# Kernel optimization log

Measured on AMD Instinct MI355X. Metric: run time of the kernel, lower is better.

Reference implementation:

```python
import jax, jax.numpy as jnp
import numpy as np

D = 512          # hidden_dim
H_HEADS = 8
DH = D // H_HEADS  # 64
L = 6            # n_layers
P = 8            # patch size
KT = 3           # temporal kernel
Z_DIM = 32
FILM_SCALE = 0.5
ROPE_BASE = 10000.0
EPS = 1e-5


def layer_norm(x, g, b):
    mu = x.mean(-1, keepdims=True)
    var = ((x - mu) ** 2).mean(-1, keepdims=True)
    return (x - mu) * jax.lax.rsqrt(var + EPS) * g + b


def rotate_half(x):
    x1, x2 = jnp.split(x, 2, axis=-1)
    return jnp.concatenate([-x2, x1], axis=-1)


def rope_time(T, dtype):
    half = DH // 2
    inv_freq = ROPE_BASE ** (-(jnp.arange(half, dtype=dtype) / half))  # (half,)
    angles = jnp.arange(T, dtype=dtype)[:, None] * inv_freq[None, :]   # (T, half)
    sin = jnp.concatenate([jnp.sin(angles), jnp.sin(angles)], -1)      # (T, DH)
    cos = jnp.concatenate([jnp.cos(angles), jnp.cos(angles)], -1)
    return sin, cos


def setup_inputs() -> dict:
    key = jax.random.key(0)
    ks = iter(jax.random.split(key, 64))
    n = lambda shape, s=0.02: jax.random.normal(next(ks), shape, jnp.float32) * s
    inp = {
        "x": jax.random.normal(next(ks), (16, 32, 3, 64, 64), jnp.float32),
        "z": jax.random.normal(next(ks), (16, 32, Z_DIM), jnp.float32),
        # tokenizer: CausalConv3d (kt,ph,pw)=(3,8,8), stride (1,8,8)
        "conv_w": n((D, 3, KT, P, P)),
        "conv_b": jnp.zeros((D,), jnp.float32),
        "tok_g": jnp.ones((D,), jnp.float32),
        "tok_b": jnp.zeros((D,), jnp.float32),
        # FiLM from z -> (gamma, beta)
        "film_w": n((Z_DIM, 2 * D)),
        "film_b": jnp.zeros((2 * D,), jnp.float32),
        # transformer blocks (stacked over L)
        "ln1_g": jnp.ones((L, D), jnp.float32), "ln1_b": jnp.zeros((L, D), jnp.float32),
        "kqv_w": n((L, D, 3 * D)), "kqv_b": jnp.zeros((L, 3 * D), jnp.float32),
        "proj_w": n((L, D, D)), "proj_b": jnp.zeros((L, D), jnp.float32),
        "ln2_g": jnp.ones((L, D), jnp.float32), "ln2_b": jnp.zeros((L, D), jnp.float32),
        "mlp_w1": n((L, D, 4 * D)), "mlp_b1": jnp.zeros((L, 4 * D), jnp.float32),
        "mlp_w2": n((L, 4 * D, D)), "mlp_b2": jnp.zeros((L, D), jnp.float32),
        "rs_attn": jnp.full((L,), 0.5, jnp.float32),
        "rs_mlp": jnp.full((L,), 0.5, jnp.float32),
        # scoring head
        "head_g": jnp.ones((D,), jnp.float32), "head_b": jnp.zeros((D,), jnp.float32),
        "head_w": n((D, 1)), "head_bias": jnp.zeros((1,), jnp.float32),
    }
    return inp


def _forward(x, z, conv_w, conv_b, tok_g, tok_b, film_w, film_b,
             ln1_g, ln1_b, kqv_w, kqv_b, proj_w, proj_b, ln2_g, ln2_b,
             mlp_w1, mlp_b1, mlp_w2, mlp_b2, rs_attn, rs_mlp,
             head_g, head_b, head_w, head_bias):
    B, T, C, Himg, Wimg = x.shape
    # ---- SpatialTemporalTokenizer: causal Conv3d (pad time on past only) ----
    xc = jnp.transpose(x, (0, 2, 1, 3, 4))  # [B,C,T,H,W]
    y = jax.lax.conv_general_dilated(
        xc, conv_w, window_strides=(1, P, P),
        padding=[(KT - 1, 0), (0, 0), (0, 0)],
        dimension_numbers=("NCDHW", "OIDHW", "NCDHW"))
    y = y + conv_b[None, :, None, None, None]          # [B,D,T,Hn,Wn]
    Hn, Wn = y.shape[3], y.shape[4]
    tok = jnp.transpose(y, (0, 2, 3, 4, 1)).reshape(B, T, Hn * Wn, D)
    tok = layer_norm(tok, tok_g, tok_b)                 # [B,T,N,D]
    # ---- FiLM conditioning from z ----
    gb = z @ film_w + film_b                            # [B,T,2D]
    gamma, beta = jnp.split(gb, 2, axis=-1)
    tok = (1.0 + FILM_SCALE * gamma)[:, :, None, :] * tok + (FILM_SCALE * beta)[:, :, None, :]
    # ---- spatial pooling -> temporal sequence ----
    h = tok.mean(axis=2)                                # [B,T,D]
    # ---- transformer stack (causal, time RoPE, pre-LN, gated residuals) ----
    sin_t, cos_t = rope_time(T, h.dtype)                # (T, DH)
    causal = jnp.tril(jnp.ones((T, T), bool))
    neg_inf = jnp.finfo(h.dtype).min
    for i in range(L):
        xi = layer_norm(h, ln1_g[i], ln1_b[i])
        kqv = xi @ kqv_w[i] + kqv_b[i]                  # [B,T,3D]
        k, q, v = jnp.split(kqv, 3, axis=-1)            # torch chunk order: k,q,v
        sh = lambda t: t.reshape(B, T, H_HEADS, DH).transpose(0, 2, 1, 3)  # [B,h,T,d]
        q, k, v = sh(q), sh(k), sh(v)
        q = q * cos_t + rotate_half(q) * sin_t
        k = k * cos_t + rotate_half(k) * sin_t
        att = jnp.einsum("bhqd,bhkd->bhqk", q, k) / np.sqrt(DH)
        att = jnp.where(causal[None, None], att, neg_inf)
        att = jax.nn.softmax(att, axis=-1)
        yv = jnp.einsum("bhqk,bhkd->bhqd", att, v)
        yv = yv.transpose(0, 2, 1, 3).reshape(B, T, D)
        attn_out = yv @ proj_w[i] + proj_b[i]
        h = h + rs_attn[i] * attn_out
        x2 = layer_norm(h, ln2_g[i], ln2_b[i])
        m = jax.nn.gelu(x2 @ mlp_w1[i] + mlp_b1[i], approximate=False) @ mlp_w2[i] + mlp_b2[i]
        h = h + rs_mlp[i] * m
    # ---- per-timestep score head ----
    h = layer_norm(h, head_g, head_b)
    score = (h @ head_w + head_bias)[..., 0]            # [B,T]
    return score


def reference(x, z, conv_w, conv_b, tok_g, tok_b, film_w, film_b,
              ln1_g, ln1_b, kqv_w, kqv_b, proj_w, proj_b, ln2_g, ln2_b,
              mlp_w1, mlp_b1, mlp_w2, mlp_b2, rs_attn, rs_mlp,
              head_g, head_b, head_w, head_bias):
    return _forward(x, z, conv_w, conv_b, tok_g, tok_b, film_w, film_b,
                    ln1_g, ln1_b, kqv_w, kqv_b, proj_w, proj_b, ln2_g, ln2_b,
                    mlp_w1, mlp_b1, mlp_w2, mlp_b2, rs_attn, rs_mlp,
                    head_g, head_b, head_w, head_bias)
```

## Files before the change

kernel.cpp:

```cpp
#include <hip/hip_runtime.h>
#include <math.h>

#define EPS 1e-5f

typedef __attribute__((ext_vector_type(8))) short short8;
typedef __attribute__((ext_vector_type(4))) float f32x4;

__device__ __forceinline__ short f2bf(float f) {
    unsigned u = __float_as_uint(f);
    u += 0x7fffu + ((u >> 16) & 1u);
    return (short)(u >> 16);
}
__device__ __forceinline__ float bf2f(short s) {
    return __uint_as_float(((unsigned)(unsigned short)s) << 16);
}
__device__ __forceinline__ void async16(const void* g, void* l) {
    __builtin_amdgcn_global_load_lds(
        (const __attribute__((address_space(1))) unsigned*)g,
        (__attribute__((address_space(3))) unsigned*)l, 16, 0, 0);
}

__device__ __forceinline__ float block_reduce_sum_256(float v, float* red) {
    #pragma unroll
    for (int o = 32; o > 0; o >>= 1) v += __shfl_down(v, o, 64);
    __syncthreads();
    if ((threadIdx.x & 63) == 0) red[threadIdx.x >> 6] = v;
    __syncthreads();
    return red[0] + red[1] + red[2] + red[3];
}

__global__ __launch_bounds__(256) void prep_all(
    const float* __restrict__ z, const float* __restrict__ fw,
    const float* __restrict__ fb, float* __restrict__ gb,
    const float* __restrict__ conv_w, short* __restrict__ wbf,
    const float* __restrict__ x, short* __restrict__ xbf,
    float* __restrict__ ropeS, float* __restrict__ ropeC,
    const float* __restrict__ kqv_w, short* __restrict__ kqvT,
    const float* __restrict__ proj_w, short* __restrict__ projT,
    const float* __restrict__ mlp_w1, short* __restrict__ mlp1T,
    const float* __restrict__ mlp_w2, short* __restrict__ mlp2T) {
    int bi = blockIdx.x, tid = threadIdx.x;
    if (bi < 512) {
        __shared__ float zs[32];
        if (tid < 32) zs[tid] = z[bi * 32 + tid];
        __syncthreads();
        for (int j = tid; j < 1024; j += 256) {
            float acc = fb[j];
            #pragma unroll
            for (int k = 0; k < 32; k++) acc = fmaf(zs[k], fw[k * 1024 + j], acc);
            gb[bi * 1024 + j] = acc;
        }
        return;
    }
    if (bi < 1664) {
        int i = (bi - 512) * 256 + tid;
        wbf[i] = f2bf(conv_w[i]);
        return;
    }
    if (bi < 4736) {
        int i = (bi - 1664) * 256 + tid;
        float4 a = *(const float4*)(x + (size_t)i * 8);
        float4 b = *(const float4*)(x + (size_t)i * 8 + 4);
        short8 o = {f2bf(a.x), f2bf(a.y), f2bf(a.z), f2bf(a.w),
                    f2bf(b.x), f2bf(b.y), f2bf(b.z), f2bf(b.w)};
        *(short8*)(xbf + (size_t)i * 8) = o;
        return;
    }
    if (bi < 4740) {
        int idx = (bi - 4736) * 256 + tid;
        if (idx < 1024) {
            int t = idx >> 5, j = idx & 31;
            float ang = (float)t * expf(-(float)j * (logf(10000.f) / 32.f));
            ropeS[idx] = sinf(ang);
            ropeC[idx] = cosf(ang);
        }
        return;
    }
    __shared__ float tile[32][33];
    int rel0 = bi - 4740;
    const float* src; short* dst; int NT, K, N, rel;
    if (rel0 < 4608)       { src = kqv_w;  dst = kqvT;  NT = 48; K = 512;  N = 1536; rel = rel0; }
    else if (rel0 < 6144)  { src = proj_w; dst = projT; NT = 16; K = 512;  N = 512;  rel = rel0 - 4608; }
    else if (rel0 < 12288) { src = mlp_w1; dst = mlp1T; NT = 64; K = 512;  N = 2048; rel = rel0 - 6144; }
    else                   { src = mlp_w2; dst = mlp2T; NT = 16; K = 2048; N = 512;  rel = rel0 - 12288; }
    int per = NT * (K / 32);
    int layer = rel / per, r2 = rel - layer * per;
    int nt = r2 % NT, kt = r2 / NT;
    src += (size_t)layer * K * N;
    dst += (size_t)layer * N * K;
    int n0 = nt * 32, k0 = kt * 32;
    int lx = tid & 31, ly = tid >> 5;
    #pragma unroll
    for (int i = 0; i < 32; i += 8)
        tile[ly + i][lx] = src[(size_t)(k0 + ly + i) * N + n0 + lx];
    __syncthreads();
    if (tid < 128) {
        int row = tid >> 2, c = tid & 3;
        short8 o;
        #pragma unroll
        for (int j = 0; j < 8; j++) o[j] = f2bf(tile[c * 8 + j][row]);
        *(short8*)(dst + (size_t)(n0 + row) * K + k0 + c * 8) = o;
    }
}

__global__ __launch_bounds__(256, 2) void conv_fused(
    const short* __restrict__ xbf, const short* __restrict__ wbf,
    const float* __restrict__ cb, const float* __restrict__ tg,
    const float* __restrict__ tb, const float* __restrict__ gb,
    float* __restrict__ h) {
    __shared__ short As[64 * 32];
    __shared__ short Bs[512 * 32];
    __shared__ float redsum[4][64], redss[4][64];
    __shared__ float mu_s[64], inv_s[64];
    int bt = blockIdx.x, b = bt >> 5, t = bt & 31;
    int tid = threadIdx.x;
    int wave = tid >> 6, lane = tid & 63, quad = lane >> 4, l16 = lane & 15;

    int rowA = tid >> 2;
    int cA = (tid & 3) ^ ((rowA >> 1) & 3);
    int hn = rowA >> 3, wn2 = rowA & 7;
    long long baseA = (((long long)(b * 32 + t - 2) * 3) << 12)
                      + (long long)(hn * 8) * 64 + wn2 * 8;

    f32x4 acc[4][8];
    #pragma unroll
    for (int mt = 0; mt < 4; mt++)
        #pragma unroll
        for (int nt = 0; nt < 8; nt++) acc[mt][nt] = (f32x4){0.f, 0.f, 0.f, 0.f};

    for (int k0 = 0; k0 < 576; k0 += 32) {
        #pragma unroll
        for (int e = 0; e < 8; e++) {
            int s = e * 256 + tid;
            int n = s >> 2;
            int c = (s & 3) ^ ((n >> 1) & 3);
            async16(wbf + (size_t)n * 576 + k0 + c * 8, Bs + s * 8);
        }
        {
            int ks = (k0 >> 3) + cA;
            int ch = (ks >= 24) + (ks >= 48);
            int r = ks - ch * 24;
            int kt = r >> 3, ph = r & 7;
            short8 v8 = (short8){0, 0, 0, 0, 0, 0, 0, 0};
            if (t + kt >= 2)
                v8 = *(const short8*)(xbf + baseA
                        + ((long long)(kt * 3 + ch) << 12) + ph * 64);
            *(short8*)(As + tid * 8) = v8;
        }
        __syncthreads();
        short8 af[4], bf[8];
        #pragma unroll
        for (int mt = 0; mt < 4; mt++) {
            int row = mt * 16 + l16;
            int pc = quad ^ ((row >> 1) & 3);
            af[mt] = *(const short8*)(As + row * 32 + pc * 8);
        }
        #pragma unroll
        for (int nt = 0; nt < 8; nt++) {
            int row = wave * 128 + nt * 16 + l16;
            int pc = quad ^ ((row >> 1) & 3);
            bf[nt] = *(const short8*)(Bs + row * 32 + pc * 8);
        }
        #pragma unroll
        for (int mt = 0; mt < 4; mt++)
            #pragma unroll
            for (int nt = 0; nt < 8; nt++)
                acc[mt][nt] = __builtin_amdgcn_mfma_f32_16x16x32_bf16(
                    af[mt], bf[nt], acc[mt][nt], 0, 0, 0);
        __syncthreads();
    }

    float cbn[8], tgn[8], tbn[8], Gn[8], Ben[8];
    #pragma unroll
    for (int nt = 0; nt < 8; nt++) {
        int n = wave * 128 + nt * 16 + l16;
        cbn[nt] = cb[n]; tgn[nt] = tg[n]; tbn[nt] = tb[n];
        Gn[nt]  = 1.f + 0.5f * gb[bt * 1024 + n];
        Ben[nt] = 0.5f * gb[bt * 1024 + 512 + n];
    }
    #pragma unroll
    for (int mt = 0; mt < 4; mt++)
        #pragma unroll
        for (int reg = 0; reg < 4; reg++) {
            float s = 0.f, ss = 0.f;
            #pragma unroll
            for (int nt = 0; nt < 8; nt++) {
                float v = acc[mt][nt][reg] + cbn[nt];
                s += v; ss += v * v;
            }
            #pragma unroll
            for (int o = 1; o < 16; o <<= 1) {
                s  += __shfl_xor(s, o, 64);
                ss += __shfl_xor(ss, o, 64);
            }
            if (l16 == 0) {
                int m = mt * 16 + quad * 4 + reg;
                redsum[wave][m] = s; redss[wave][m] = ss;
            }
        }
    __syncthreads();
    if (tid < 64) {
        float S  = redsum[0][tid] + redsum[1][tid] + redsum[2][tid] + redsum[3][tid];
        float SS = redss[0][tid] + redss[1][tid] + redss[2][tid] + redss[3][tid];
        float mu = S * (1.f / 512.f);
        float var = SS * (1.f / 512.f) - mu * mu;
        mu_s[tid] = mu; inv_s[tid] = rsqrtf(var + EPS);
    }
    __syncthreads();
    float hacc[8] = {0.f, 0.f, 0.f, 0.f, 0.f, 0.f, 0.f, 0.f};
    #pragma unroll
    for (int mt = 0; mt < 4; mt++)
        #pragma unroll
        for (int reg = 0; reg < 4; reg++) {
            int m = mt * 16 + quad * 4 + reg;
            float mu = mu_s[m], inv = inv_s[m];
            #pragma unroll
            for (int nt = 0; nt < 8; nt++) {
                float v = acc[mt][nt][reg] + cbn[nt];
                hacc[nt] += (v - mu) * inv;
            }
        }
    #pragma unroll
    for (int nt = 0; nt < 8; nt++) {
        hacc[nt] += __shfl_xor(hacc[nt], 16, 64);
        hacc[nt] += __shfl_xor(hacc[nt], 32, 64);
    }
    if (quad == 0)
        #pragma unroll
        for (int nt = 0; nt < 8; nt++) {
            int n = wave * 128 + nt * 16 + l16;
            h[bt * 512 + n] = Gn[nt] * (tgn[nt] * (hacc[nt] * (1.f / 64.f)) + tbn[nt])
                              + Ben[nt];
        }
}

__global__ __launch_bounds__(256) void attn_fused(
    const float* __restrict__ hsrc, const float* __restrict__ lng,
    const float* __restrict__ lnb, const short* __restrict__ Bw,
    const float* __restrict__ bias, const float* __restrict__ ropeS,
    const float* __restrict__ ropeC, short* __restrict__ yv) {
    __shared__ char smem[57344] __attribute__((aligned(16)));
    __shared__ float mu_s[32], inv_s[32];
    short* As = (short*)smem;
    short* BsB[2] = {(short*)(smem + 32768), (short*)(smem + 45056)};
    float (*qsf)[64] = (float(*)[64])(smem);
    float (*ksf)[64] = (float(*)[64])(smem + 8192);
    short* vT  = (short*)(smem + 16384);
    short* qrb = (short*)(smem + 20480);
    short* krb = (short*)(smem + 24576);
    float (*att)[33] = (float(*)[33])(smem + 28672);
    short* pA  = (short*)(smem + 36864);
    int blk = blockIdx.x, b = blk >> 3, hh = blk & 7;
    int tid = threadIdx.x;
    int m0 = b * 32;
    {
        int row = tid >> 3, l8 = tid & 7;
        const float* hp = hsrc + (size_t)(m0 + row) * 512 + l8 * 64;
        float s = 0.f, ss = 0.f;
        #pragma unroll
        for (int i = 0; i < 16; i++) {
            float4 v = *(const float4*)(hp + i * 4);
            s += v.x + v.y + v.z + v.w;
            ss += v.x * v.x + v.y * v.y + v.z * v.z + v.w * v.w;
        }
        s += __shfl_xor(s, 1, 64); ss += __shfl_xor(ss, 1, 64);
        s += __shfl_xor(s, 2, 64); ss += __shfl_xor(ss, 2, 64);
        s += __shfl_xor(s, 4, 64); ss += __shfl_xor(ss, 4, 64);
        if (l8 == 0) {
            float mu = s * (1.f / 512.f);
            float var = ss * (1.f / 512.f) - mu * mu;
            mu_s[row] = mu;
            inv_s[row] = rsqrtf(var + EPS);
        }
    }
    #pragma unroll
    for (int e = 0; e < 3; e++) {
        int p = e * 256 + tid;
        int row = p >> 2, seg = (p & 3) ^ ((row >> 1) & 3);
        int n = ((row >> 6) << 9) + hh * 64 + (row & 63);
        async16(Bw + (size_t)n * 512 + seg * 8, BsB[0] + p * 8);
    }
    __syncthreads();
    #pragma unroll
    for (int e = 0; e < 8; e++) {
        int lc = e * 256 + tid;
        int row = lc >> 6, cc = lc & 63;
        float mu = mu_s[row], inv = inv_s[row];
        const float* hp = hsrc + (size_t)(m0 + row) * 512 + cc * 8;
        float4 a = *(const float4*)hp, b2 = *(const float4*)(hp + 4);
        float4 g0 = *(const float4*)(lng + cc * 8), g1 = *(const float4*)(lng + cc * 8 + 4);
        float4 b0 = *(const float4*)(lnb + cc * 8), b1 = *(const float4*)(lnb + cc * 8 + 4);
        short8 o = {f2bf((a.x - mu) * inv * g0.x + b0.x),
                    f2bf((a.y - mu) * inv * g0.y + b0.y),
                    f2bf((a.z - mu) * inv * g0.z + b0.z),
                    f2bf((a.w - mu) * inv * g0.w + b0.w),
                    f2bf((b2.x - mu) * inv * g1.x + b1.x),
                    f2bf((b2.y - mu) * inv * g1.y + b1.y),
                    f2bf((b2.z - mu) * inv * g1.z + b1.z),
                    f2bf((b2.w - mu) * inv * g1.w + b1.w)};
        *(short8*)(As + (row * 64 + (cc ^ (row & 7))) * 8) = o;
    }
    __syncthreads();
    int wave = tid >> 6, lane = tid & 63, quad = lane >> 4, l16 = lane & 15;
    f32x4 acc[2][3];
    #pragma unroll
    for (int m2 = 0; m2 < 2; m2++)
        #pragma unroll
        for (int g = 0; g < 3; g++) acc[m2][g] = (f32x4){0.f, 0.f, 0.f, 0.f};
    for (int it = 0; it < 16; it++) {
        short* Bsc = BsB[it & 1];
        if (it < 15) {
            int k0n = (it + 1) * 32;
            short* Bsn = BsB[(it + 1) & 1];
            #pragma unroll
            for (int e = 0; e < 3; e++) {
                int p = e * 256 + tid;
                int row = p >> 2, seg = (p & 3) ^ ((row >> 1) & 3);
                int n = ((row >> 6) << 9) + hh * 64 + (row & 63);
                async16(Bw + (size_t)n * 512 + k0n + seg * 8, Bsn + p * 8);
            }
        }
        int cc = it * 4 + quad;
        short8 af[2], bf[3];
        #pragma unroll
        for (int m2 = 0; m2 < 2; m2++) {
            int row = m2 * 16 + l16;
            af[m2] = *(const short8*)(As + (row * 64 + (cc ^ (row & 7))) * 8);
        }
        #pragma unroll
        for (int g = 0; g < 3; g++) {
            int row = g * 64 + wave * 16 + l16;
            int pc = quad ^ ((row >> 1) & 3);
            bf[g] = *(const short8*)(Bsc + (row * 4 + pc) * 8);
        }
        #pragma unroll
        for (int m2 = 0; m2 < 2; m2++)
            #pragma unroll
            for (int g = 0; g < 3; g++)
                acc[m2][g] = __builtin_amdgcn_mfma_f32_16x16x32_bf16(
                    af[m2], bf[g], acc[m2][g], 0, 0, 0);
        __syncthreads();
    }
    float bb0 = bias[hh * 64 + wave * 16 + l16];
    float bb1 = bias[512 + hh * 64 + wave * 16 + l16];
    float bb2 = bias[1024 + hh * 64 + wave * 16 + l16];
    int dcol = wave * 16 + l16;
    #pragma unroll
    for (int m2 = 0; m2 < 2; m2++)
        #pragma unroll
        for (int reg = 0; reg < 4; reg++) {
            int tkn = m2 * 16 + quad * 4 + reg;
            ksf[tkn][dcol] = acc[m2][0][reg] + bb0;
            qsf[tkn][dcol] = acc[m2][1][reg] + bb1;
            vT[dcol * 32 + (((tkn >> 3) ^ (dcol & 3)) << 3) + (tkn & 7)]
                = f2bf(acc[m2][2][reg] + bb2);
        }
    __syncthreads();
    #pragma unroll
    for (int e = 0; e < 8; e++) {
        int idx = e * 256 + tid;
        int t = idx >> 6, d = idx & 63, j = d & 31;
        float sv = ropeS[t * 32 + j], cv = ropeC[t * 32 + j];
        float qv = qsf[t][d], kv = ksf[t][d];
        float qo = qsf[t][d ^ 32], ko = ksf[t][d ^ 32];
        float rq = (d < 32) ? -qo : qo;
        float rk = (d < 32) ? -ko : ko;
        int addr = t * 64 + (((d >> 3) ^ (t & 7)) << 3) + (d & 7);
        qrb[addr] = f2bf(qv * cv + rq * sv);
        krb[addr] = f2bf(kv * cv + rk * sv);
    }
    __syncthreads();
    int mw = wave & 1, nw = wave >> 1;
    {
        f32x4 sc = (f32x4){0.f, 0.f, 0.f, 0.f};
        #pragma unroll
        for (int kc = 0; kc < 2; kc++) {
            int rq = mw * 16 + l16;
            int rk = nw * 16 + l16;
            short8 aq = *(const short8*)(qrb + rq * 64 + ((((kc << 2) + quad) ^ (rq & 7)) << 3));
            short8 bk = *(const short8*)(krb + rk * 64 + ((((kc << 2) + quad) ^ (rk & 7)) << 3));
            sc = __builtin_amdgcn_mfma_f32_16x16x32_bf16(aq, bk, sc, 0, 0, 0);
        }
        #pragma unroll
        for (int reg = 0; reg < 4; reg++) {
            int qt = mw * 16 + quad * 4 + reg;
            int kt = nw * 16 + l16;
            att[qt][kt] = (kt > qt) ? -1e30f : sc[reg] * 0.125f;
        }
    }
    __syncthreads();
    {
        int row = tid >> 3, g = tid & 7;
        float v0 = att[row][g * 4], v1 = att[row][g * 4 + 1];
        float v2 = att[row][g * 4 + 2], v3 = att[row][g * 4 + 3];
        float mx = fmaxf(fmaxf(v0, v1), fmaxf(v2, v3));
        mx = fmaxf(mx, __shfl_xor(mx, 1, 64));
        mx = fmaxf(mx, __shfl_xor(mx, 2, 64));
        mx = fmaxf(mx, __shfl_xor(mx, 4, 64));
        float e0 = expf(v0 - mx), e1 = expf(v1 - mx);
        float e2 = expf(v2 - mx), e3 = expf(v3 - mx);
        float s = e0 + e1 + e2 + e3;
        s += __shfl_xor(s, 1, 64);
        s += __shfl_xor(s, 2, 64);
        s += __shfl_xor(s, 4, 64);
        float inv = 1.f / s;
        short* pp = pA + row * 32 + g * 4;
        pp[0] = f2bf(e0 * inv); pp[1] = f2bf(e1 * inv);
        pp[2] = f2bf(e2 * inv); pp[3] = f2bf(e3 * inv);
    }
    __syncthreads();
    {
        int rp = mw * 16 + l16;
        short8 ap = *(const short8*)(pA + rp * 32 + quad * 8);
        #pragma unroll
        for (int i = 0; i < 2; i++) {
            int nt = (wave >> 1) * 2 + i;
            int rv = nt * 16 + l16;
            short8 bv = *(const short8*)(vT + rv * 32 + (((quad ^ (rv & 3))) << 3));
            f32x4 o = (f32x4){0.f, 0.f, 0.f, 0.f};
            o = __builtin_amdgcn_mfma_f32_16x16x32_bf16(ap, bv, o, 0, 0, 0);
            #pragma unroll
            for (int reg = 0; reg < 4; reg++) {
                int t = mw * 16 + quad * 4 + reg;
                int d = nt * 16 + l16;
                yv[(size_t)(b * 32 + t) * 512 + hh * 64 + d] = f2bf(o[reg]);
            }
        }
    }
}

__global__ __launch_bounds__(256) void gemm_ln(
    const float* __restrict__ hsrc, const float* __restrict__ lng,
    const float* __restrict__ lnb, const short* __restrict__ Bw,
    const float* __restrict__ bias, int N, int mode,
    float* __restrict__ outf, short* __restrict__ outb) {
    __shared__ short As[32 * 512];
    __shared__ short Bs[128 * 128];
    __shared__ float mu_s[32], inv_s[32];
    int tid = threadIdx.x;
    int m0 = blockIdx.y * 32, n0 = blockIdx.x * 128;
    {
        int row = tid >> 3, l8 = tid & 7;
        const float* hp = hsrc + (size_t)(m0 + row) * 512 + l8 * 64;
        float s = 0.f, ss = 0.f;
        #pragma unroll
        for (int i = 0; i < 16; i++) {
            float4 v = *(const float4*)(hp + i * 4);
            s += v.x + v.y + v.z + v.w;
            ss += v.x * v.x + v.y * v.y + v.z * v.z + v.w * v.w;
        }
        s += __shfl_xor(s, 1, 64); ss += __shfl_xor(ss, 1, 64);
        s += __shfl_xor(s, 2, 64); ss += __shfl_xor(ss, 2, 64);
        s += __shfl_xor(s, 4, 64); ss += __shfl_xor(ss, 4, 64);
        if (l8 == 0) {
            float mu = s * (1.f / 512.f);
            float var = ss * (1.f / 512.f) - mu * mu;
            mu_s[row] = mu;
            inv_s[row] = rsqrtf(var + EPS);
        }
    }
    #pragma unroll
    for (int e = 0; e < 8; e++) {
        int p = e * 256 + tid;
        int row = p >> 4, seg = (p & 15) ^ (row & 15);
        async16(Bw + (size_t)(n0 + row) * 512 + seg * 8, Bs + p * 8);
    }
    __syncthreads();
    #pragma unroll
    for (int e = 0; e < 8; e++) {
        int lc = e * 256 + tid;
        int row = lc >> 6, cc = lc & 63;
        float mu = mu_s[row], inv = inv_s[row];
        const float* hp = hsrc + (size_t)(m0 + row) * 512 + cc * 8;
        float4 a = *(const float4*)hp, b = *(const float4*)(hp + 4);
        float4 g0 = *(const float4*)(lng + cc * 8), g1 = *(const float4*)(lng + cc * 8 + 4);
        float4 b0 = *(const float4*)(lnb + cc * 8), b1 = *(const float4*)(lnb + cc * 8 + 4);
        short8 o = {f2bf((a.x - mu) * inv * g0.x + b0.x),
                    f2bf((a.y - mu) * inv * g0.y + b0.y),
                    f2bf((a.z - mu) * inv * g0.z + b0.z),
                    f2bf((a.w - mu) * inv * g0.w + b0.w),
                    f2bf((b.x - mu) * inv * g1.x + b1.x),
                    f2bf((b.y - mu) * inv * g1.y + b1.y),
                    f2bf((b.z - mu) * inv * g1.z + b1.z),
                    f2bf((b.w - mu) * inv * g1.w + b1.w)};
        *(short8*)(As + (row * 64 + (cc ^ (row & 7))) * 8) = o;
    }
    __syncthreads();
    int wave = tid >> 6, lane = tid & 63, quad = lane >> 4, l16 = lane & 15;
    f32x4 acc[2][2];
    #pragma unroll
    for (int a2 = 0; a2 < 2; a2++)
        #pragma unroll
        for (int b2 = 0; b2 < 2; b2++) acc[a2][b2] = (f32x4){0.f, 0.f, 0.f, 0.f};
    for (int it = 0; it < 4; it++) {
        int k0 = it * 128;
        #pragma unroll
        for (int ksub = 0; ksub < 4; ksub++) {
            int ccb = ksub * 4 + quad;
            short8 af[2], bf[2];
            #pragma unroll
            for (int m2 = 0; m2 < 2; m2++) {
                int row = m2 * 16 + l16;
                int cc = (k0 >> 3) + ccb;
                af[m2] = *(const short8*)(As + (row * 64 + (cc ^ (row & 7))) * 8);
            }
            #pragma unroll
            for (int n2 = 0; n2 < 2; n2++) {
                int row = wave * 32 + n2 * 16 + l16;
                bf[n2] = *(const short8*)(Bs + (row * 16 + (ccb ^ (row & 15))) * 8);
            }
            #pragma unroll
            for (int m2 = 0; m2 < 2; m2++)
                #pragma unroll
                for (int n2 = 0; n2 < 2; n2++)
                    acc[m2][n2] = __builtin_amdgcn_mfma_f32_16x16x32_bf16(
                        af[m2], bf[n2], acc[m2][n2], 0, 0, 0);
        }
        __syncthreads();
        if (it < 3) {
            int k0n = (it + 1) * 128;
            #pragma unroll
            for (int e = 0; e < 8; e++) {
                int p = e * 256 + tid;
                int row = p >> 4, seg = (p & 15) ^ (row & 15);
                async16(Bw + (size_t)(n0 + row) * 512 + k0n + seg * 8, Bs + p * 8);
            }
            __syncthreads();
        }
    }
    #pragma unroll
    for (int m2 = 0; m2 < 2; m2++)
        #pragma unroll
        for (int n2 = 0; n2 < 2; n2++)
            #pragma unroll
            for (int reg = 0; reg < 4; reg++) {
                int m = m0 + m2 * 16 + quad * 4 + reg;
                int n = n0 + wave * 32 + n2 * 16 + l16;
                float v = acc[m2][n2][reg] + bias[n];
                if (mode == 1) {
                    v = 0.5f * v * (1.f + erff(v * 0.70710678118f));
                    outb[(size_t)m * N + n] = f2bf(v);
                } else {
                    outf[(size_t)m * N + n] = v;
                }
            }
}

__global__ __launch_bounds__(256) void gemm_res(
    const short* __restrict__ Ag, const short* __restrict__ Bw,
    const float* __restrict__ bias, const float* __restrict__ rsPtr,
    float* __restrict__ hm, int K, int Ks) {
    __shared__ short As[2][32 * 128];
    __shared__ short Bs[2][64 * 128];
    int tid = threadIdx.x;
    int m0 = blockIdx.y * 32, n0 = blockIdx.x * 64;
    int kbase = blockIdx.z * Ks;
    int wave = tid >> 6, lane = tid & 63, quad = lane >> 4, l16 = lane & 15;
    int nIter = Ks >> 7;
    f32x4 acc[2];
    acc[0] = (f32x4){0.f, 0.f, 0.f, 0.f};
    acc[1] = (f32x4){0.f, 0.f, 0.f, 0.f};
    auto stage = [&](int k0, int buf) {
        #pragma unroll
        for (int e = 0; e < 2; e++) {
            int p = e * 256 + tid;
            int row = p >> 4, seg = (p & 15) ^ (row & 15);
            async16(Ag + (size_t)(m0 + row) * K + k0 + seg * 8, As[buf] + p * 8);
        }
        #pragma unroll
        for (int e = 0; e < 4; e++) {
            int p = e * 256 + tid;
            int row = p >> 4, seg = (p & 15) ^ (row & 15);
            async16(Bw + (size_t)(n0 + row) * K + k0 + seg * 8, Bs[buf] + p * 8);
        }
    };
    stage(kbase, 0);
    __syncthreads();
    for (int it = 0; it < nIter; it++) {
        int cur = it & 1;
        if (it + 1 < nIter) stage(kbase + (it + 1) * 128, cur ^ 1);
        #pragma unroll
        for (int ksub = 0; ksub < 4; ksub++) {
            int ccb = ksub * 4 + quad;
            short8 bf;
            {
                int row = wave * 16 + l16;
                bf = *(const short8*)(Bs[cur] + (row * 16 + (ccb ^ (row & 15))) * 8);
            }
            #pragma unroll
            for (int m2 = 0; m2 < 2; m2++) {
                int row = m2 * 16 + l16;
                short8 af = *(const short8*)(As[cur] + (row * 16 + (ccb ^ (row & 15))) * 8);
                acc[m2] = __builtin_amdgcn_mfma_f32_16x16x32_bf16(af, bf, acc[m2], 0, 0, 0);
            }
        }
        __syncthreads();
    }
    float rsv = *rsPtr;
    bool addb = (blockIdx.z == 0);
    #pragma unroll
    for (int m2 = 0; m2 < 2; m2++)
        #pragma unroll
        for (int reg = 0; reg < 4; reg++) {
            int m = m0 + m2 * 16 + quad * 4 + reg;
            int n = n0 + wave * 16 + l16;
            float v = acc[m2][reg] + (addb ? bias[n] : 0.f);
            atomicAdd(&hm[(size_t)m * 512 + n], rsv * v);
        }
}

__global__ __launch_bounds__(256) void head_kernel(
    const float* __restrict__ h, const float* __restrict__ g,
    const float* __restrict__ bb, const float* __restrict__ w,
    const float* __restrict__ bias0, float* __restrict__ out) {
    __shared__ float red[8];
    int token = blockIdx.x, tid = threadIdx.x;
    float v0 = h[token * 512 + tid], v1 = h[token * 512 + tid + 256];
    float s  = block_reduce_sum_256(v0 + v1, red);
    float ss = block_reduce_sum_256(v0 * v0 + v1 * v1, red);
    float mu = s * (1.f / 512.f);
    float var = ss * (1.f / 512.f) - mu * mu;
    float inv = rsqrtf(var + EPS);
    float n0 = (v0 - mu) * inv * g[tid] + bb[tid];
    float n1 = (v1 - mu) * inv * g[tid + 256] + bb[tid + 256];
    float dot = block_reduce_sum_256(n0 * w[tid] + n1 * w[tid + 256], red);
    if (tid == 0) out[token] = dot + bias0[0];
}

extern "C" void kernel_launch(void* const* d_in, const int* in_sizes, int n_in,
                              void* d_out, int out_size, void* d_ws, size_t ws_size,
                              hipStream_t stream) {
    const float* x       = (const float*)d_in[0];
    const float* z       = (const float*)d_in[1];
    const float* conv_w  = (const float*)d_in[2];
    const float* conv_b  = (const float*)d_in[3];
    const float* tok_g   = (const float*)d_in[4];
    const float* tok_b   = (const float*)d_in[5];
    const float* film_w  = (const float*)d_in[6];
    const float* film_b  = (const float*)d_in[7];
    const float* ln1_g   = (const float*)d_in[8];
    const float* ln1_b   = (const float*)d_in[9];
    const float* kqv_w   = (const float*)d_in[10];
    const float* kqv_b   = (const float*)d_in[11];
    const float* proj_w  = (const float*)d_in[12];
    const float* proj_b  = (const float*)d_in[13];
    const float* ln2_g   = (const float*)d_in[14];
    const float* ln2_b   = (const float*)d_in[15];
    const float* mlp_w1  = (const float*)d_in[16];
    const float* mlp_b1  = (const float*)d_in[17];
    const float* mlp_w2  = (const float*)d_in[18];
    const float* mlp_b2  = (const float*)d_in[19];
    const float* rs_attn = (const float*)d_in[20];
    const float* rs_mlp  = (const float*)d_in[21];
    const float* head_g  = (const float*)d_in[22];
    const float* head_b  = (const float*)d_in[23];
    const float* head_w  = (const float*)d_in[24];
    const float* head_bs = (const float*)d_in[25];
    float* out = (float*)d_out;

    float* ws = (float*)d_ws;
    float* gb    = ws;
    float* h     = gb + 524288;
    float* ropeS = h + 262144;
    float* ropeC = ropeS + 1024;
    short* sb = (short*)(ropeC + 1024);
    short* wbf   = sb;
    short* kqvT  = wbf   + 294912;
    short* projT = kqvT  + 4718592;
    short* mlp1T = projT + 1572864;
    short* mlp2T = mlp1T + 6291456;
    short* yvb   = mlp2T + 6291456;
    short* mbuf  = yvb   + 262144;
    short* xbf   = mbuf  + 1048576;

    prep_all<<<23172, 256, 0, stream>>>(
        z, film_w, film_b, gb, conv_w, wbf, x, xbf, ropeS, ropeC,
        kqv_w, kqvT, proj_w, projT, mlp_w1, mlp1T, mlp_w2, mlp2T);

    conv_fused<<<512, 256, 0, stream>>>(xbf, wbf, conv_b, tok_g, tok_b, gb, h);

    for (int i = 0; i < 6; i++) {
        attn_fused<<<128, 256, 0, stream>>>(
            h, ln1_g + i * 512, ln1_b + i * 512,
            kqvT + (size_t)i * 1536 * 512, kqv_b + i * 1536, ropeS, ropeC, yvb);
        gemm_res<<<dim3(8, 16, 2), 256, 0, stream>>>(
            yvb, projT + (size_t)i * 512 * 512, proj_b + i * 512,
            rs_attn + i, h, 512, 256);
        gemm_ln<<<dim3(16, 16), 256, 0, stream>>>(
            h, ln2_g + i * 512, ln2_b + i * 512,
            mlp1T + (size_t)i * 2048 * 512, mlp_b1 + i * 2048,
            2048, 1, nullptr, mbuf);
        gemm_res<<<dim3(8, 16, 4), 256, 0, stream>>>(
            mbuf, mlp2T + (size_t)i * 512 * 2048, mlp_b2 + i * 512,
            rs_mlp + i, h, 2048, 512);
    }

    head_kernel<<<512, 256, 0, stream>>>(h, head_g, head_b, head_w, head_bs, out);
}
```

Baseline: 465.1 us.

## Merge transformer layer loop into persistent megakernel with grid barriers

Replaces the 24 per-layer kernel launches plus the head launch with a single persistent 256-workgroup kernel that runs the attention, projection, MLP1 and MLP2 phases in sequence, separated by atomic-counter grid barriers. The aim is to remove launch gaps and tail effects between the many small kernels. Because the grid is fixed at 256 workgroups, the phases are re-split: the MLP2 split-K drops from 4 to 2 and the attention phase uses only 128 of the 256 workgroups. The spin barrier relies on all workgroups being co-resident, and it has a timeout that could silently break synchronization if that does not hold.

```diff
diff --git a/kernel.cpp b/kernel.cpp
--- a/kernel.cpp
+++ b/kernel.cpp
@@ -18,6 +18,21 @@
     __builtin_amdgcn_global_load_lds(
         (const __attribute__((address_space(1))) unsigned*)g,
         (__attribute__((address_space(3))) unsigned*)l, 16, 0, 0);
+}
+
+__device__ __forceinline__ void gsync(unsigned* bar, unsigned goal) {
+    __syncthreads();
+    if (threadIdx.x == 0) {
+        __threadfence();
+        __hip_atomic_fetch_add(bar, 1u, __ATOMIC_RELAXED, __HIP_MEMORY_SCOPE_AGENT);
+        unsigned spins = 0;
+        while (__hip_atomic_load(bar, __ATOMIC_RELAXED, __HIP_MEMORY_SCOPE_AGENT) < goal) {
+            __builtin_amdgcn_s_sleep(2);
+            if (++spins > 20000000u) break;
+        }
+        __threadfence();
+    }
+    __syncthreads();
 }
 
 __device__ __forceinline__ float block_reduce_sum_256(float v, float* red) {
@@ -38,8 +53,10 @@
     const float* __restrict__ kqv_w, short* __restrict__ kqvT,
     const float* __restrict__ proj_w, short* __restrict__ projT,
     const float* __restrict__ mlp_w1, short* __restrict__ mlp1T,
-    const float* __restrict__ mlp_w2, short* __restrict__ mlp2T) {
+    const float* __restrict__ mlp_w2, short* __restrict__ mlp2T,
+    unsigned* __restrict__ bar) {
     int bi = blockIdx.x, tid = threadIdx.x;
+    if (bi == 0 && tid == 0) *bar = 0u;
     if (bi < 512) {
         __shared__ float zs[32];
         if (tid < 32) zs[tid] = z[bi * 32 + tid];
@@ -234,13 +251,15 @@
         }
 }
 
-__global__ __launch_bounds__(256) void attn_fused(
+
+__device__ __forceinline__ void attn_phase(
+    char* smem, int blk, int tid,
     const float* __restrict__ hsrc, const float* __restrict__ lng,
     const float* __restrict__ lnb, const short* __restrict__ Bw,
     const float* __restrict__ bias, const float* __restrict__ ropeS,
     const float* __restrict__ ropeC, short* __restrict__ yv) {
-    __shared__ char smem[57344] __attribute__((aligned(16)));
-    __shared__ float mu_s[32], inv_s[32];
+    float* mu_s = (float*)(smem + 65536);
+    float* inv_s = (float*)(smem + 65664);
     short* As = (short*)smem;
     short* BsB[2] = {(short*)(smem + 32768), (short*)(smem + 45056)};
     float (*qsf)[64] = (float(*)[64])(smem);
@@ -250,8 +269,7 @@
     short* krb = (short*)(smem + 24576);
     float (*att)[33] = (float(*)[33])(smem + 28672);
     short* pA  = (short*)(smem + 36864);
-    int blk = blockIdx.x, b = blk >> 3, hh = blk & 7;
-    int tid = threadIdx.x;
+    int b = blk >> 3, hh = blk & 7;
     int m0 = b * 32;
     {
         int row = tid >> 3, l8 = tid & 7;
@@ -427,18 +445,19 @@
             }
         }
     }
-}
-
-__global__ __launch_bounds__(256) void gemm_ln(
+    __syncthreads();
+}
+
+__device__ __forceinline__ void gemm_ln_phase(
+    char* smem, int bx, int by, int tid,
     const float* __restrict__ hsrc, const float* __restrict__ lng,
     const float* __restrict__ lnb, const short* __restrict__ Bw,
-    const float* __restrict__ bias, int N, int mode,
-    float* __restrict__ outf, short* __restrict__ outb) {
-    __shared__ short As[32 * 512];
-    __shared__ short Bs[128 * 128];
-    __shared__ float mu_s[32], inv_s[32];
-    int tid = threadIdx.x;
-    int m0 = blockIdx.y * 32, n0 = blockIdx.x * 128;
+    const float* __restrict__ bias, int N, short* __restrict__ outb) {
+    short* As = (short*)smem;
+    short* Bs = (short*)(smem + 32768);
+    float* mu_s = (float*)(smem + 65536);
+    float* inv_s = (float*)(smem + 65664);
+    int m0 = by * 32, n0 = bx * 128;
     {
         int row = tid >> 3, l8 = tid & 7;
         const float* hp = hsrc + (size_t)(m0 + row) * 512 + l8 * 64;
@@ -537,24 +556,21 @@
                 int m = m0 + m2 * 16 + quad * 4 + reg;
                 int n = n0 + wave * 32 + n2 * 16 + l16;
                 float v = acc[m2][n2][reg] + bias[n];
-                if (mode == 1) {
-                    v = 0.5f * v * (1.f + erff(v * 0.70710678118f));
-                    outb[(size_t)m * N + n] = f2bf(v);
-                } else {
-                    outf[(size_t)m * N + n] = v;
-                }
-            }
-}
-
-__global__ __launch_bounds__(256) void gemm_res(
+                v = 0.5f * v * (1.f + erff(v * 0.70710678118f));
+                outb[(size_t)m * N + n] = f2bf(v);
+            }
+    __syncthreads();
+}
+
+__device__ __forceinline__ void gemm_res_phase(
+    char* smem, int bx, int by, int bz, int tid,
     const short* __restrict__ Ag, const short* __restrict__ Bw,
     const float* __restrict__ bias, const float* __restrict__ rsPtr,
     float* __restrict__ hm, int K, int Ks) {
-    __shared__ short As[2][32 * 128];
-    __shared__ short Bs[2][64 * 128];
-    int tid = threadIdx.x;
-    int m0 = blockIdx.y * 32, n0 = blockIdx.x * 64;
-    int kbase = blockIdx.z * Ks;
+    short* As = (short*)smem;
+    short* Bs = (short*)(smem + 16384);
+    int m0 = by * 32, n0 = bx * 64;
+    int kbase = bz * Ks;
     int wave = tid >> 6, lane = tid & 63, quad = lane >> 4, l16 = lane & 15;
     int nIter = Ks >> 7;
     f32x4 acc[2];
@@ -565,13 +581,13 @@
         for (int e = 0; e < 2; e++) {
             int p = e * 256 + tid;
             int row = p >> 4, seg = (p & 15) ^ (row & 15);
-            async16(Ag + (size_t)(m0 + row) * K + k0 + seg * 8, As[buf] + p * 8);
+            async16(Ag + (size_t)(m0 + row) * K + k0 + seg * 8, As + buf * 4096 + p * 8);
         }
         #pragma unroll
         for (int e = 0; e < 4; e++) {
             int p = e * 256 + tid;
             int row = p >> 4, seg = (p & 15) ^ (row & 15);
-            async16(Bw + (size_t)(n0 + row) * K + k0 + seg * 8, Bs[buf] + p * 8);
+            async16(Bw + (size_t)(n0 + row) * K + k0 + seg * 8, Bs + buf * 8192 + p * 8);
         }
     };
     stage(kbase, 0);
@@ -585,19 +601,19 @@
             short8 bf;
             {
                 int row = wave * 16 + l16;
-                bf = *(const short8*)(Bs[cur] + (row * 16 + (ccb ^ (row & 15))) * 8);
+                bf = *(const short8*)(Bs + cur * 8192 + (row * 16 + (ccb ^ (row & 15))) * 8);
             }
             #pragma unroll
             for (int m2 = 0; m2 < 2; m2++) {
                 int row = m2 * 16 + l16;
-                short8 af = *(const short8*)(As[cur] + (row * 16 + (ccb ^ (row & 15))) * 8);
+                short8 af = *(const short8*)(As + cur * 4096 + (row * 16 + (ccb ^ (row & 15))) * 8);
                 acc[m2] = __builtin_amdgcn_mfma_f32_16x16x32_bf16(af, bf, acc[m2], 0, 0, 0);
             }
         }
         __syncthreads();
     }
     float rsv = *rsPtr;
-    bool addb = (blockIdx.z == 0);
+    bool addb = (bz == 0);
     #pragma unroll
     for (int m2 = 0; m2 < 2; m2++)
         #pragma unroll
@@ -609,12 +625,12 @@
         }
 }
 
-__global__ __launch_bounds__(256) void head_kernel(
+__device__ __forceinline__ void head_phase(
+    char* smem, int token, int tid,
     const float* __restrict__ h, const float* __restrict__ g,
     const float* __restrict__ bb, const float* __restrict__ w,
     const float* __restrict__ bias0, float* __restrict__ out) {
-    __shared__ float red[8];
-    int token = blockIdx.x, tid = threadIdx.x;
+    float* red = (float*)smem;
     float v0 = h[token * 512 + tid], v1 = h[token * 512 + tid + 256];
     float s  = block_reduce_sum_256(v0 + v1, red);
     float ss = block_reduce_sum_256(v0 * v0 + v1 * v1, red);
@@ -625,6 +641,53 @@
     float n1 = (v1 - mu) * inv * g[tid + 256] + bb[tid + 256];
     float dot = block_reduce_sum_256(n0 * w[tid] + n1 * w[tid + 256], red);
     if (tid == 0) out[token] = dot + bias0[0];
+}
+
+__global__ __launch_bounds__(256) void mega(
+    float* __restrict__ h, short* __restrict__ yvb, short* __restrict__ mbuf,
+    const float* __restrict__ ropeS, const float* __restrict__ ropeC,
+    const short* __restrict__ kqvT, const short* __restrict__ projT,
+    const short* __restrict__ mlp1T, const short* __restrict__ mlp2T,
+    const float* __restrict__ ln1_g, const float* __restrict__ ln1_b,
+    const float* __restrict__ kqv_b, const float* __restrict__ proj_b,
+    const float* __restrict__ ln2_g, const float* __restrict__ ln2_b,
+    const float* __restrict__ mlp_b1, const float* __restrict__ mlp_b2,
+    const float* __restrict__ rs_attn, const float* __restrict__ rs_mlp,
+    const float* __restrict__ head_g, const float* __restrict__ head_b,
+    const float* __restrict__ head_w, const float* __restrict__ head_bs,
+    float* __restrict__ out, unsigned* __restrict__ bar) {
+    __shared__ char smem[65792] __attribute__((aligned(16)));
+    int wg = blockIdx.x, tid = threadIdx.x;
+    unsigned sgoal = 0;
+
+    for (int i = 0; i < 6; i++) {
+        if (wg < 128)
+            attn_phase(smem, wg, tid, h, ln1_g + i * 512, ln1_b + i * 512,
+                       kqvT + (size_t)i * 786432, kqv_b + i * 1536,
+                       ropeS, ropeC, yvb);
+        sgoal += 256; gsync(bar, sgoal);
+        {
+            int bz = wg >> 7, r = wg & 127;
+            gemm_res_phase(smem, r & 7, r >> 3, bz, tid, yvb,
+                           projT + (size_t)i * 262144, proj_b + i * 512,
+                           rs_attn + i, h, 512, 256);
+        }
+        sgoal += 256; gsync(bar, sgoal);
+        gemm_ln_phase(smem, wg & 15, wg >> 4, tid, h,
+                      ln2_g + i * 512, ln2_b + i * 512,
+                      mlp1T + (size_t)i * 1048576, mlp_b1 + i * 2048,
+                      2048, mbuf);
+        sgoal += 256; gsync(bar, sgoal);
+        {
+            int bz = wg >> 7, r = wg & 127;
+            gemm_res_phase(smem, r & 7, r >> 3, bz, tid, mbuf,
+                           mlp2T + (size_t)i * 1048576, mlp_b2 + i * 512,
+                           rs_mlp + i, h, 2048, 1024);
+        }
+        sgoal += 256; gsync(bar, sgoal);
+    }
+    head_phase(smem, wg * 2, tid, h, head_g, head_b, head_w, head_bs, out);
+    head_phase(smem, wg * 2 + 1, tid, h, head_g, head_b, head_w, head_bs, out);
 }
 
 extern "C" void kernel_launch(void* const* d_in, const int* in_sizes, int n_in,
@@ -672,28 +735,16 @@
     short* yvb   = mlp2T + 6291456;
     short* mbuf  = yvb   + 262144;
     short* xbf   = mbuf  + 1048576;
+    unsigned* bar = (unsigned*)(xbf + 6291456);
 
     prep_all<<<23172, 256, 0, stream>>>(
         z, film_w, film_b, gb, conv_w, wbf, x, xbf, ropeS, ropeC,
-        kqv_w, kqvT, proj_w, projT, mlp_w1, mlp1T, mlp_w2, mlp2T);
+        kqv_w, kqvT, proj_w, projT, mlp_w1, mlp1T, mlp_w2, mlp2T, bar);
 
     conv_fused<<<512, 256, 0, stream>>>(xbf, wbf, conv_b, tok_g, tok_b, gb, h);
 
-    for (int i = 0; i < 6; i++) {
-        attn_fused<<<128, 256, 0, stream>>>(
-            h, ln1_g + i * 512, ln1_b + i * 512,
-            kqvT + (size_t)i * 1536 * 512, kqv_b + i * 1536, ropeS, ropeC, yvb);
-        gemm_res<<<dim3(8, 16, 2), 256, 0, stream>>>(
-            yvb, projT + (size_t)i * 512 * 512, proj_b + i * 512,
-            rs_attn + i, h, 512, 256);
-        gemm_ln<<<dim3(16, 16), 256, 0, stream>>>(
-            h, ln2_g + i * 512, ln2_b + i * 512,
-            mlp1T + (size_t)i * 2048 * 512, mlp_b1 + i * 2048,
-            2048, 1, nullptr, mbuf);
-        gemm_res<<<dim3(8, 16, 4), 256, 0, stream>>>(
-            mbuf, mlp2T + (size_t)i * 512 * 2048, mlp_b2 + i * 512,
-            rs_mlp + i, h, 2048, 512);
-    }
-
-    head_kernel<<<512, 256, 0, stream>>>(h, head_g, head_b, head_w, head_bs, out);
-}
+    mega<<<256, 256, 0, stream>>>(
+        h, yvb, mbuf, ropeS, ropeC, kqvT, projT, mlp1T, mlp2T,
+        ln1_g, ln1_b, kqv_b, proj_b, ln2_g, ln2_b, mlp_b1, mlp_b2,
+        rs_attn, rs_mlp, head_g, head_b, head_w, head_bs, out, bar);
+}
```

Result: slower. 834.0 us (+79.3%).
